# Optimization experiments

Measured on AMD Instinct MI355X. Metric: run time of the kernel, lower is better.

## Reference

```python
import jax, jax.numpy as jnp
import numpy as np

B, S, D = 1, 2048, 2048
E, K, F = 16, 4, 512
EPS = 1e-6


def setup_inputs() -> dict:
    key = jax.random.key(0)
    ks = jax.random.split(key, 5)
    return {
        "hidden_states": jax.random.normal(ks[0], (B, S, D), dtype=jnp.float32),
        "norm_weight": jnp.ones((D,), dtype=jnp.float32),
        "gate_w": jax.random.normal(ks[1], (E, D), dtype=jnp.float32) * 0.02,
        "w_gate": jax.random.normal(ks[2], (E, D, F), dtype=jnp.float32) * 0.02,
        "w_up": jax.random.normal(ks[3], (E, D, F), dtype=jnp.float32) * 0.02,
        "w_down": jax.random.normal(ks[4], (E, F, D), dtype=jnp.float32) * 0.02,
    }


def _rmsnorm(x, w, eps=EPS):
    xf = x.astype(jnp.float32)
    var = jnp.mean(xf * xf, axis=-1, keepdims=True)
    return (xf * jax.lax.rsqrt(var + eps)).astype(x.dtype) * w


def reference(hidden_states, norm_weight, gate_w, w_gate, w_up, w_down):
    residual = hidden_states
    h = _rmsnorm(hidden_states, norm_weight)
    x = h.reshape(-1, D)                                  # [T, D], T = B*S
    T = x.shape[0]

    # Router: softmax over experts (fp32), top-k, renormalize top-k weights.
    logits = x @ gate_w.T                                  # [T, E]
    probs = jax.nn.softmax(logits.astype(jnp.float32), axis=-1)
    top_w, top_i = jax.lax.top_k(probs, K)                 # [T, K]
    top_w = top_w / jnp.sum(top_w, axis=-1, keepdims=True)
    top_w = top_w.astype(x.dtype)

    # Dense combine matrix [T, E]: routing weight if selected, else 0.
    comb = jnp.zeros((T, E), dtype=x.dtype)
    comb = comb.at[jnp.arange(T)[:, None], top_i].add(top_w)

    # Experts: SiLU-gated MLP per expert, combined with routing weights.
    g = jnp.einsum("td,edf->tef", x, w_gate)               # [T, E, F]
    u = jnp.einsum("td,edf->tef", x, w_up)                 # [T, E, F]
    act = jax.nn.silu(g) * u                               # [T, E, F]
    # Weight per-expert contributions then project down.
    y = jnp.einsum("tef,efd,te->td", act, w_down, comb)    # [T, D]

    out = residual + y.reshape(B, S, D)
    return out
```

## Files before the change

### kernel.cpp

```cpp
#include <hip/hip_runtime.h>
#include <cstdint>
#include <cstddef>

#define T_ 2048
#define D_ 2048
#define E_ 16
#define F_ 512

typedef unsigned short u16;
typedef unsigned int u32;
typedef unsigned long long u64;
typedef __attribute__((ext_vector_type(8))) short bf16x8;
typedef __attribute__((ext_vector_type(4))) float f32x4;
typedef __attribute__((ext_vector_type(2))) u32 u32x2;
typedef __attribute__((ext_vector_type(4))) u32 u32x4;
typedef __attribute__((ext_vector_type(8))) u16 u16x8;

__device__ __forceinline__ u16 f2bf(float f){
  union { float f; u32 u; } c; c.f = f;
  return (u16)((c.u + 0x7FFFu + ((c.u >> 16) & 1u)) >> 16);
}

__device__ __forceinline__ void gload16(const void* g, void* l){
  __builtin_amdgcn_global_load_lds((const __attribute__((address_space(1))) void*)g,
                                   (__attribute__((address_space(3))) void*)l,
                                   16, 0, 0);
}

__device__ __forceinline__ u32 pk2(float a, float b){
  u32 r;
  asm("v_cvt_pk_bf16_f32 %0, %1, %2" : "=v"(r) : "v"(a), "v"(b));
  return r;
}

__global__ __launch_bounds__(256) void k_norm_router(
    const float* __restrict__ x, const float* __restrict__ nw, const float* __restrict__ gw,
    u16* __restrict__ h, int* __restrict__ tok_e, float* __restrict__ tok_w)
{
  const int t = blockIdx.x, tid = threadIdx.x;
  const int lane = tid & 63, wid = tid >> 6;
  const int d0 = tid * 8;
  const float4 v0 = *(const float4*)(x + (size_t)t*D_ + d0);
  const float4 v1 = *(const float4*)(x + (size_t)t*D_ + d0 + 4);
  float hv[8] = {v0.x, v0.y, v0.z, v0.w, v1.x, v1.y, v1.z, v1.w};
  float ss = 0.f;
  #pragma unroll
  for (int j = 0; j < 8; ++j) ss += hv[j]*hv[j];
  #pragma unroll
  for (int o = 32; o; o >>= 1) ss += __shfl_xor(ss, o);
  __shared__ float sred[4];
  __shared__ float red16[4][16];
  __shared__ float lf[16];
  if (lane == 0) sred[wid] = ss;
  __syncthreads();
  const float rstd = rsqrtf((sred[0]+sred[1]+sred[2]+sred[3]) * (1.f/(float)D_) + 1e-6f);
  const float4 w0 = *(const float4*)(nw + d0);
  const float4 w1 = *(const float4*)(nw + d0 + 4);
  const float wv[8] = {w0.x,w0.y,w0.z,w0.w,w1.x,w1.y,w1.z,w1.w};
  #pragma unroll
  for (int j = 0; j < 8; ++j) hv[j] = hv[j] * rstd * wv[j];
  u16x8 hb;
  #pragma unroll
  for (int j = 0; j < 8; ++j) hb[j] = f2bf(hv[j]);
  *(u16x8*)(h + (size_t)t*D_ + d0) = hb;

  float lg[16];
  #pragma unroll
  for (int e = 0; e < 16; ++e){
    const float4 g0 = *(const float4*)(gw + e*D_ + d0);
    const float4 g1 = *(const float4*)(gw + e*D_ + d0 + 4);
    lg[e] = hv[0]*g0.x + hv[1]*g0.y + hv[2]*g0.z + hv[3]*g0.w
          + hv[4]*g1.x + hv[5]*g1.y + hv[6]*g1.z + hv[7]*g1.w;
  }
  #pragma unroll
  for (int e = 0; e < 16; ++e){
    #pragma unroll
    for (int o = 32; o; o >>= 1) lg[e] += __shfl_xor(lg[e], o);
  }
  if (lane == 0){
    #pragma unroll
    for (int e = 0; e < 16; ++e) red16[wid][e] = lg[e];
  }
  __syncthreads();
  if (tid < 16) lf[tid] = red16[0][tid] + red16[1][tid] + red16[2][tid] + red16[3][tid];
  __syncthreads();
  if (tid == 0){
    float l[16];
    #pragma unroll
    for (int e = 0; e < 16; ++e) l[e] = lf[e];
    int sel[4]; float sv[4]; u32 used = 0;
    for (int k = 0; k < 4; ++k){
      float b = -3.4e38f; int bi = 0;
      for (int e = 0; e < 16; ++e)
        if (!((used >> e) & 1u) && l[e] > b){ b = l[e]; bi = e; }
      used |= 1u << bi; sel[k] = bi; sv[k] = b;
    }
    float ex[4]; float s = 0.f;
    for (int k = 0; k < 4; ++k){ ex[k] = __expf(sv[k] - sv[0]); s += ex[k]; }
    const float inv = 1.f / s;
    int4 te = {sel[0], sel[1], sel[2], sel[3]};
    float4 tw4 = {ex[0]*inv, ex[1]*inv, ex[2]*inv, ex[3]*inv};
    *(int4*)(tok_e + t*4) = te;
    *(float4*)(tok_w + t*4) = tw4;
  }
}

__global__ __launch_bounds__(256) void k_build_lists(
    const int* __restrict__ tok_e, const float* __restrict__ tok_w,
    int* __restrict__ eidx, float* __restrict__ ew, int* __restrict__ counts)
{
  const int e = blockIdx.x, tid = threadIdx.x;
  const int lane = tid & 63, wid = tid >> 6;
  __shared__ int wtot[4];
  __shared__ int base;
  if (tid == 0) base = 0;
  __syncthreads();
  for (int t0 = 0; t0 < T_; t0 += 256){
    const int t = t0 + tid;
    const int4 te = *(const int4*)(tok_e + t*4);
    const float4 tw = *(const float4*)(tok_w + t*4);
    bool m = false; float wv = 0.f;
    if      (te.x == e){ m = true; wv = tw.x; }
    else if (te.y == e){ m = true; wv = tw.y; }
    else if (te.z == e){ m = true; wv = tw.z; }
    else if (te.w == e){ m = true; wv = tw.w; }
    const u64 mask = __ballot(m);
    const int pre = __popcll(mask & ((1ull << lane) - 1ull));
    if (lane == 0) wtot[wid] = __popcll(mask);
    __syncthreads();
    int wbase = base;
    for (int i = 0; i < wid; ++i) wbase += wtot[i];
    if (m){
      eidx[e*T_ + wbase + pre] = t;
      ew[e*T_ + wbase + pre] = wv;
    }
    __syncthreads();
    if (tid == 0) base += wtot[0] + wtot[1] + wtot[2] + wtot[3];
    __syncthreads();
  }
  if (tid == 0) counts[e] = base;
}

__global__ __launch_bounds__(256) void k_slots(
    const int* __restrict__ counts, const int* __restrict__ eidx,
    const int* __restrict__ tok_e, int* __restrict__ tok_slot)
{
  const int e = blockIdx.x;
  int abase = 0;
  for (int i = 0; i < e; ++i) abase += counts[i];
  const int cnt = counts[e];
  for (int s = threadIdx.x; s < cnt; s += 256){
    const int t = eidx[e*T_ + s];
    const int4 te = *(const int4*)(tok_e + t*4);
    const int kidx = (te.x == e) ? 0 : (te.y == e) ? 1 : (te.z == e) ? 2 : 3;
    tok_slot[t*4 + kidx] = abase + s;
  }
}

#define WLOAD(KB, SRC, S) do {                                                 \
    _Pragma("unroll")                                                          \
    for (int j = 0; j < 2; ++j){                                               \
      const float4 t_ = *(const float4*)((SRC) + (size_t)((KB) + ko*2 + j)*(S));\
      wvf[0][j]=t_.x; wvf[1][j]=t_.y; wvf[2][j]=t_.z; wvf[3][j]=t_.w;          \
    }                                                                          \
  } while (0)

#define WSTORE(WP) do {                                                        \
    _Pragma("unroll")                                                          \
    for (int i = 0; i < 4; ++i){                                               \
      const int r_ = rg4*4 + i;                                                \
      const u32 idx_ = (u32)(r_*32 + ((ko>>2) ^ (r_&3) ^ ((r_>>2)&3))*8 + (ko&3)*2); \
      *(u32*)&(WP)[idx_] = pk2(wvf[i][0], wvf[i][1]);                          \
    }                                                                          \
  } while (0)

__global__ __launch_bounds__(256, 4) void k_gateup(
    const u16* __restrict__ h, const float* __restrict__ wg, const float* __restrict__ wu,
    const int* __restrict__ counts, const int* __restrict__ eidx, const float* __restrict__ ew,
    u16* __restrict__ act)
{
  const int bid = blockIdx.x;
  const int tt = bid >> 8;
  const int e  = (bid >> 4) & 15;
  const int ft = bid & 15;

  const int cnt = counts[e];
  const int row0 = tt * 256;
  if (row0 >= cnt) return;
  int abase = 0;
  for (int i = 0; i < e; ++i) abase += counts[i];

  const int tid = threadIdx.x, lane = tid & 63, w = tid >> 6;
  const int f0 = ft * 32;

  __shared__ __align__(16) u16 Xs[3][8192];
  __shared__ __align__(16) u16 Ws[2][2048];

  int* toksS = (int*)&Xs[0][0];
  if (tid < 256){
    const int slot = row0 + tid;
    const int cs = slot < cnt ? slot : (cnt - 1);
    toksS[tid] = eidx[e*T_ + cs];
  }
  __syncthreads();

  const int lr = lane >> 2, lc = lane & 3;
  const int csw = lc ^ (lr & 3) ^ ((lr >> 2) & 3);
  const u16* srcX[4]; u32 dof[4];
  #pragma unroll
  for (int q = 0; q < 4; ++q){
    const int r = w*64 + q*16 + lr;
    srcX[q] = h + (size_t)toksS[r]*D_ + 8*csw;
    dof[q] = (u32)((w*64 + q*16) * 32);
  }
  const int rg4 = tid & 15, ko = tid >> 4;
  const float* wsel = (rg4 < 8) ? wg : wu;
  const float* srcWf = wsel + (size_t)e*D_*F_ + f0 + ((rg4*4) & 31);
  __syncthreads();

  const int p = lane & 15, g4 = lane >> 4;
  u32 aB[4], bB[4];
  #pragma unroll
  for (int m = 0; m < 4; ++m) aB[m] = (u32)((w*64 + m*16 + p) * 32);
  #pragma unroll
  for (int n = 0; n < 4; ++n) bB[n] = (u32)((n*16 + p) * 32);
  const u32 s8 = 8u * (u32)(g4 ^ (p & 3) ^ ((p >> 2) & 3));

  f32x4 acc[4][4] = {};
  float wvf[4][2];

  WLOAD(0, srcWf, F_);
  #pragma unroll
  for (int q = 0; q < 4; ++q) gload16(srcX[q],      (void*)&Xs[0][dof[q]]);
  #pragma unroll
  for (int q = 0; q < 4; ++q) gload16(srcX[q] + 32, (void*)&Xs[1][dof[q]]);
  asm volatile("s_waitcnt vmcnt(8)" ::: "memory");
  __builtin_amdgcn_sched_barrier(0);
  WSTORE(&Ws[0][0]);
  asm volatile("s_waitcnt vmcnt(4)" ::: "memory");

  const int NSTEP = D_ / 32;
  int xc = 0;
  for (int kt = 0; kt < NSTEP; ++kt){
    asm volatile("s_waitcnt lgkmcnt(0)" ::: "memory");
    __builtin_amdgcn_s_barrier();
    __builtin_amdgcn_sched_barrier(0);
    if (kt + 1 < NSTEP){
      WLOAD((kt + 1) * 32, srcWf, F_);
      __builtin_amdgcn_sched_barrier(0);
    }
    {
      const u16* Xp = &Xs[xc][0];
      const u16* Wp = &Ws[kt & 1][0];
      bf16x8 aF[4], bF[4];
      #pragma unroll
      for (int m = 0; m < 4; ++m) aF[m] = *(const bf16x8*)&Xp[aB[m] + s8];
      #pragma unroll
      for (int n = 0; n < 4; ++n) bF[n] = *(const bf16x8*)&Wp[bB[n] + s8];
      #pragma unroll
      for (int m = 0; m < 4; ++m)
        #pragma unroll
        for (int n = 0; n < 4; ++n)
          acc[m][n] = __builtin_amdgcn_mfma_f32_16x16x32_bf16(aF[m], bF[n], acc[m][n], 0, 0, 0);
    }
    if (kt + 2 < NSTEP){
      const int kb2 = (kt + 2) * 32;
      int nb = xc + 2; if (nb >= 3) nb -= 3;
      #pragma unroll
      for (int q = 0; q < 4; ++q) gload16(srcX[q] + kb2, (void*)&Xs[nb][dof[q]]);
    }
    if (kt + 1 < NSTEP){
      if (kt + 2 < NSTEP) asm volatile("s_waitcnt vmcnt(4)" ::: "memory");
      else                asm volatile("s_waitcnt vmcnt(0)" ::: "memory");
      __builtin_amdgcn_sched_barrier(0);
      WSTORE(&Ws[(kt + 1) & 1][0]);
    }
    xc = (xc == 2) ? 0 : xc + 1;
  }

  #pragma unroll
  for (int m = 0; m < 4; ++m)
    #pragma unroll
    for (int r = 0; r < 4; ++r){
      const int row  = w*64 + m*16 + g4*4 + r;
      const int slot = row0 + row;
      if (slot < cnt){
        const float tw = ew[e*T_ + slot];
        #pragma unroll
        for (int n = 0; n < 2; ++n){
          const float gv = acc[m][n][r], uv = acc[m][n+2][r];
          const float a = tw * (gv / (1.f + __expf(-gv))) * uv;
          act[(size_t)(abase + slot)*F_ + f0 + n*16 + p] = f2bf(a);
        }
      }
    }
}

__global__ __launch_bounds__(512, 4) void k_down(
    const u16* __restrict__ act, const float* __restrict__ wd,
    const int* __restrict__ counts, u16* __restrict__ ydown)
{
  const int bid = blockIdx.x;
  const int tt = bid >> 8;
  const int e  = (bid >> 4) & 15;
  const int dt = bid & 15;

  const int cnt = counts[e], row0 = tt * 256;
  if (row0 >= cnt) return;
  int abase = 0;
  for (int i = 0; i < e; ++i) abase += counts[i];

  const int tid = threadIdx.x, lane = tid & 63, w = tid >> 6;
  const int d0 = dt * 128;

  __shared__ __align__(16) u16 As[3][8192];
  __shared__ __align__(16) u16 Wd[2][4096];

  const int lr = lane >> 2, lc = lane & 3;
  const int csw = lc ^ (lr & 3) ^ ((lr >> 2) & 3);
  const u16* srcX[2]; u32 dof[2];
  #pragma unroll
  for (int q = 0; q < 2; ++q){
    const int r = w*32 + q*16 + lr;
    const int rs = (row0 + r < cnt) ? (row0 + r) : (cnt - 1);
    srcX[q] = act + (size_t)(abase + rs)*F_ + 8*csw;
    dof[q] = (u32)((w*32 + q*16) * 32);
  }
  const int rg4 = tid & 31, ko = tid >> 5;
  const float* srcWf = wd + (size_t)e*F_*D_ + d0 + rg4*4;

  const int p = lane & 15, g4 = lane >> 4;
  const int tm = w >> 1, dh = w & 1;
  u32 aB[4], bB[4];
  #pragma unroll
  for (int m = 0; m < 4; ++m) aB[m] = (u32)((tm*64 + m*16 + p) * 32);
  #pragma unroll
  for (int n = 0; n < 4; ++n) bB[n] = (u32)((dh*64 + n*16 + p) * 32);
  const u32 s8 = 8u * (u32)(g4 ^ (p & 3) ^ ((p >> 2) & 3));

  f32x4 acc[4][4] = {};
  float wvf[4][2];

  WLOAD(0, srcWf, D_);
  #pragma unroll
  for (int q = 0; q < 2; ++q) gload16(srcX[q],      (void*)&As[0][dof[q]]);
  #pragma unroll
  for (int q = 0; q < 2; ++q) gload16(srcX[q] + 32, (void*)&As[1][dof[q]]);
  asm volatile("s_waitcnt vmcnt(4)" ::: "memory");
  __builtin_amdgcn_sched_barrier(0);
  WSTORE(&Wd[0][0]);
  asm volatile("s_waitcnt vmcnt(2)" ::: "memory");

  const int NSTEP = F_ / 32;
  int xc = 0;
  for (int kt = 0; kt < NSTEP; ++kt){
    asm volatile("s_waitcnt lgkmcnt(0)" ::: "memory");
    __builtin_amdgcn_s_barrier();
    __builtin_amdgcn_sched_barrier(0);
    if (kt + 1 < NSTEP){
      WLOAD((kt + 1) * 32, srcWf, D_);
      __builtin_amdgcn_sched_barrier(0);
    }
    {
      const u16* Ap = &As[xc][0];
      const u16* Wp = &Wd[kt & 1][0];
      bf16x8 aF[4], bF[4];
      #pragma unroll
      for (int m = 0; m < 4; ++m) aF[m] = *(const bf16x8*)&Ap[aB[m] + s8];
      #pragma unroll
      for (int n = 0; n < 4; ++n) bF[n] = *(const bf16x8*)&Wp[bB[n] + s8];
      #pragma unroll
      for (int m = 0; m < 4; ++m)
        #pragma unroll
        for (int n = 0; n < 4; ++n)
          acc[m][n] = __builtin_amdgcn_mfma_f32_16x16x32_bf16(aF[m], bF[n], acc[m][n], 0, 0, 0);
    }
    if (kt + 2 < NSTEP){
      const int kb2 = (kt + 2) * 32;
      int nb = xc + 2; if (nb >= 3) nb -= 3;
      #pragma unroll
      for (int q = 0; q < 2; ++q) gload16(srcX[q] + kb2, (void*)&As[nb][dof[q]]);
    }
    if (kt + 1 < NSTEP){
      if (kt + 2 < NSTEP) asm volatile("s_waitcnt vmcnt(2)" ::: "memory");
      else                asm volatile("s_waitcnt vmcnt(0)" ::: "memory");
      __builtin_amdgcn_sched_barrier(0);
      WSTORE(&Wd[(kt + 1) & 1][0]);
    }
    xc = (xc == 2) ? 0 : xc + 1;
  }

  #pragma unroll
  for (int m = 0; m < 4; ++m){
    #pragma unroll
    for (int r = 0; r < 4; ++r){
      const int row  = tm*64 + m*16 + g4*4 + r;
      const int slot = row0 + row;
      if (slot < cnt){
        u16* yp = ydown + (size_t)(abase + slot)*D_ + d0 + dh*64;
        #pragma unroll
        for (int n = 0; n < 4; ++n)
          yp[n*16 + p] = f2bf(acc[m][n][r]);
      }
    }
  }
}

__global__ __launch_bounds__(256) void k_combine(
    const float* __restrict__ x, const u16* __restrict__ ydown,
    const int* __restrict__ tok_slot, float* __restrict__ out)
{
  const int t = blockIdx.x;
  const int d0 = threadIdx.x * 8;
  const int4 sl = *(const int4*)(tok_slot + t*4);
  const float4 x0 = *(const float4*)(x + (size_t)t*D_ + d0);
  const float4 x1 = *(const float4*)(x + (size_t)t*D_ + d0 + 4);
  float s[8] = {x0.x, x0.y, x0.z, x0.w, x1.x, x1.y, x1.z, x1.w};
  const int sls[4] = {sl.x, sl.y, sl.z, sl.w};
  #pragma unroll
  for (int k = 0; k < 4; ++k){
    const u16x8 v = *(const u16x8*)(ydown + (size_t)sls[k]*D_ + d0);
    #pragma unroll
    for (int j = 0; j < 8; ++j){
      union { u32 u; float f; } c; c.u = (u32)v[j] << 16;
      s[j] += c.f;
    }
  }
  float4 o0 = {s[0], s[1], s[2], s[3]};
  float4 o1 = {s[4], s[5], s[6], s[7]};
  *(float4*)(out + (size_t)t*D_ + d0)     = o0;
  *(float4*)(out + (size_t)t*D_ + d0 + 4) = o1;
}

extern "C" void kernel_launch(void* const* d_in, const int* in_sizes, int n_in,
                              void* d_out, int out_size, void* d_ws, size_t ws_size,
                              hipStream_t stream)
{
  (void)in_sizes; (void)n_in; (void)out_size; (void)ws_size;
  const float* x     = (const float*)d_in[0];
  const float* nw    = (const float*)d_in[1];
  const float* gw    = (const float*)d_in[2];
  const float* wgate = (const float*)d_in[3];
  const float* wup   = (const float*)d_in[4];
  const float* wdown = (const float*)d_in[5];
  float* out = (float*)d_out;

  char* ws = (char*)d_ws;
  u16*   h        = (u16*)(ws);
  u16*   act      = (u16*)(ws + 8388608);
  int*   counts   = (int*)(ws + 16908288);
  int*   eidx     = (int*)(ws + 16908352);
  float* ew       = (float*)(ws + 17039424);
  int*   tok_e    = (int*)(ws + 17170496);
  float* tok_w    = (float*)(ws + 17203264);
  int*   tok_slot = (int*)(ws + 17236032);
  u16*   ydown    = (u16*)(ws + 17268800);

  k_norm_router<<<T_, 256, 0, stream>>>(x, nw, gw, h, tok_e, tok_w);
  k_build_lists<<<E_, 256, 0, stream>>>(tok_e, tok_w, eidx, ew, counts);
  k_slots<<<E_, 256, 0, stream>>>(counts, eidx, tok_e, tok_slot);
  k_gateup<<<2048, 256, 0, stream>>>(h, wgate, wup, counts, eidx, ew, act);
  k_down<<<2048, 512, 0, stream>>>(act, wdown, counts, ydown);
  k_combine<<<T_, 256, 0, stream>>>(x, ydown, tok_slot, out);
}
```

Measured before the change: 205.0 us.

## Widen gate/up tile to 64 F-columns with 8-wave blocks

The gate/up kernel now uses 512-thread blocks that each cover 256 tokens by 64 F columns (gate and up), with warps split 4x2 over rows and F halves. This halves the number of blocks and the gathered activation rows loaded per output column, so each X tile in shared memory is reused across twice as many weight columns. The weight tile buffer doubles, and each thread issues fewer X gathers per step. The trade-off is fewer blocks in flight and higher per-block shared memory, which may lower occupancy. The load/store macros are renamed, with no change in behavior.

```diff
diff --git a/kernel.cpp b/kernel.cpp
--- a/kernel.cpp
+++ b/kernel.cpp
@@ -157,7 +157,7 @@
   }
 }
 
-#define WLOAD(KB, SRC, S) do {                                                 \
+#define WLOADD(KB, SRC, S) do {                                                \
     _Pragma("unroll")                                                          \
     for (int j = 0; j < 2; ++j){                                               \
       const float4 t_ = *(const float4*)((SRC) + (size_t)((KB) + ko*2 + j)*(S));\
@@ -165,7 +165,7 @@
     }                                                                          \
   } while (0)
 
-#define WSTORE(WP) do {                                                        \
+#define WSTORED(WP) do {                                                       \
     _Pragma("unroll")                                                          \
     for (int i = 0; i < 4; ++i){                                               \
       const int r_ = rg4*4 + i;                                                \
@@ -174,15 +174,15 @@
     }                                                                          \
   } while (0)
 
-__global__ __launch_bounds__(256, 4) void k_gateup(
+__global__ __launch_bounds__(512, 4) void k_gateup(
     const u16* __restrict__ h, const float* __restrict__ wg, const float* __restrict__ wu,
     const int* __restrict__ counts, const int* __restrict__ eidx, const float* __restrict__ ew,
     u16* __restrict__ act)
 {
   const int bid = blockIdx.x;
-  const int tt = bid >> 8;
-  const int e  = (bid >> 4) & 15;
-  const int ft = bid & 15;
+  const int tt = bid >> 7;
+  const int e  = (bid >> 3) & 15;
+  const int ft = bid & 7;
 
   const int cnt = counts[e];
   const int row0 = tt * 256;
@@ -191,10 +191,10 @@
   for (int i = 0; i < e; ++i) abase += counts[i];
 
   const int tid = threadIdx.x, lane = tid & 63, w = tid >> 6;
-  const int f0 = ft * 32;
+  const int f0 = ft * 64;
 
   __shared__ __align__(16) u16 Xs[3][8192];
-  __shared__ __align__(16) u16 Ws[2][2048];
+  __shared__ __align__(16) u16 Ws[2][4096];
 
   int* toksS = (int*)&Xs[0][0];
   if (tid < 256){
@@ -206,38 +206,42 @@
 
   const int lr = lane >> 2, lc = lane & 3;
   const int csw = lc ^ (lr & 3) ^ ((lr >> 2) & 3);
-  const u16* srcX[4]; u32 dof[4];
-  #pragma unroll
-  for (int q = 0; q < 4; ++q){
-    const int r = w*64 + q*16 + lr;
+  const u16* srcX[2]; u32 dof[2];
+  #pragma unroll
+  for (int q = 0; q < 2; ++q){
+    const int r = w*32 + q*16 + lr;
     srcX[q] = h + (size_t)toksS[r]*D_ + 8*csw;
-    dof[q] = (u32)((w*64 + q*16) * 32);
-  }
-  const int rg4 = tid & 15, ko = tid >> 4;
-  const float* wsel = (rg4 < 8) ? wg : wu;
-  const float* srcWf = wsel + (size_t)e*D_*F_ + f0 + ((rg4*4) & 31);
+    dof[q] = (u32)((w*32 + q*16) * 32);
+  }
+  const int rg4 = tid & 31, ko = tid >> 5;
+  const float* wsel = (rg4 < 16) ? wg : wu;
+  const float* srcWf = wsel + (size_t)e*D_*F_ + f0 + ((rg4*4) & 63);
   __syncthreads();
 
   const int p = lane & 15, g4 = lane >> 4;
+  const int tm = w >> 1, fh = w & 1;
   u32 aB[4], bB[4];
   #pragma unroll
-  for (int m = 0; m < 4; ++m) aB[m] = (u32)((w*64 + m*16 + p) * 32);
-  #pragma unroll
-  for (int n = 0; n < 4; ++n) bB[n] = (u32)((n*16 + p) * 32);
+  for (int m = 0; m < 4; ++m) aB[m] = (u32)((tm*64 + m*16 + p) * 32);
+  #pragma unroll
+  for (int n = 0; n < 2; ++n){
+    bB[n]   = (u32)((     fh*32 + n*16 + p) * 32);
+    bB[n+2] = (u32)((64 + fh*32 + n*16 + p) * 32);
+  }
   const u32 s8 = 8u * (u32)(g4 ^ (p & 3) ^ ((p >> 2) & 3));
 
   f32x4 acc[4][4] = {};
   float wvf[4][2];
 
-  WLOAD(0, srcWf, F_);
-  #pragma unroll
-  for (int q = 0; q < 4; ++q) gload16(srcX[q],      (void*)&Xs[0][dof[q]]);
-  #pragma unroll
-  for (int q = 0; q < 4; ++q) gload16(srcX[q] + 32, (void*)&Xs[1][dof[q]]);
-  asm volatile("s_waitcnt vmcnt(8)" ::: "memory");
+  WLOADD(0, srcWf, F_);
+  #pragma unroll
+  for (int q = 0; q < 2; ++q) gload16(srcX[q],      (void*)&Xs[0][dof[q]]);
+  #pragma unroll
+  for (int q = 0; q < 2; ++q) gload16(srcX[q] + 32, (void*)&Xs[1][dof[q]]);
+  asm volatile("s_waitcnt vmcnt(4)" ::: "memory");
   __builtin_amdgcn_sched_barrier(0);
-  WSTORE(&Ws[0][0]);
-  asm volatile("s_waitcnt vmcnt(4)" ::: "memory");
+  WSTORED(&Ws[0][0]);
+  asm volatile("s_waitcnt vmcnt(2)" ::: "memory");
 
   const int NSTEP = D_ / 32;
   int xc = 0;
@@ -246,7 +250,7 @@
     __builtin_amdgcn_s_barrier();
     __builtin_amdgcn_sched_barrier(0);
     if (kt + 1 < NSTEP){
-      WLOAD((kt + 1) * 32, srcWf, F_);
+      WLOADD((kt + 1) * 32, srcWf, F_);
       __builtin_amdgcn_sched_barrier(0);
     }
     {
@@ -267,13 +271,13 @@
       const int kb2 = (kt + 2) * 32;
       int nb = xc + 2; if (nb >= 3) nb -= 3;
       #pragma unroll
-      for (int q = 0; q < 4; ++q) gload16(srcX[q] + kb2, (void*)&Xs[nb][dof[q]]);
+      for (int q = 0; q < 2; ++q) gload16(srcX[q] + kb2, (void*)&Xs[nb][dof[q]]);
     }
     if (kt + 1 < NSTEP){
-      if (kt + 2 < NSTEP) asm volatile("s_waitcnt vmcnt(4)" ::: "memory");
+      if (kt + 2 < NSTEP) asm volatile("s_waitcnt vmcnt(2)" ::: "memory");
       else                asm volatile("s_waitcnt vmcnt(0)" ::: "memory");
       __builtin_amdgcn_sched_barrier(0);
-      WSTORE(&Ws[(kt + 1) & 1][0]);
+      WSTORED(&Ws[(kt + 1) & 1][0]);
     }
     xc = (xc == 2) ? 0 : xc + 1;
   }
@@ -282,7 +286,7 @@
   for (int m = 0; m < 4; ++m)
     #pragma unroll
     for (int r = 0; r < 4; ++r){
-      const int row  = w*64 + m*16 + g4*4 + r;
+      const int row  = tm*64 + m*16 + g4*4 + r;
       const int slot = row0 + row;
       if (slot < cnt){
         const float tw = ew[e*T_ + slot];
@@ -290,7 +294,7 @@
         for (int n = 0; n < 2; ++n){
           const float gv = acc[m][n][r], uv = acc[m][n+2][r];
           const float a = tw * (gv / (1.f + __expf(-gv))) * uv;
-          act[(size_t)(abase + slot)*F_ + f0 + n*16 + p] = f2bf(a);
+          act[(size_t)(abase + slot)*F_ + f0 + fh*32 + n*16 + p] = f2bf(a);
         }
       }
     }
@@ -341,14 +345,14 @@
   f32x4 acc[4][4] = {};
   float wvf[4][2];
 
-  WLOAD(0, srcWf, D_);
+  WLOADD(0, srcWf, D_);
   #pragma unroll
   for (int q = 0; q < 2; ++q) gload16(srcX[q],      (void*)&As[0][dof[q]]);
   #pragma unroll
   for (int q = 0; q < 2; ++q) gload16(srcX[q] + 32, (void*)&As[1][dof[q]]);
   asm volatile("s_waitcnt vmcnt(4)" ::: "memory");
   __builtin_amdgcn_sched_barrier(0);
-  WSTORE(&Wd[0][0]);
+  WSTORED(&Wd[0][0]);
   asm volatile("s_waitcnt vmcnt(2)" ::: "memory");
 
   const int NSTEP = F_ / 32;
@@ -358,7 +362,7 @@
     __builtin_amdgcn_s_barrier();
     __builtin_amdgcn_sched_barrier(0);
     if (kt + 1 < NSTEP){
-      WLOAD((kt + 1) * 32, srcWf, D_);
+      WLOADD((kt + 1) * 32, srcWf, D_);
       __builtin_amdgcn_sched_barrier(0);
     }
     {
@@ -385,7 +389,7 @@
       if (kt + 2 < NSTEP) asm volatile("s_waitcnt vmcnt(2)" ::: "memory");
       else                asm volatile("s_waitcnt vmcnt(0)" ::: "memory");
       __builtin_amdgcn_sched_barrier(0);
-      WSTORE(&Wd[(kt + 1) & 1][0]);
+      WSTORED(&Wd[(kt + 1) & 1][0]);
     }
     xc = (xc == 2) ? 0 : xc + 1;
   }
@@ -459,7 +463,7 @@
   k_norm_router<<<T_, 256, 0, stream>>>(x, nw, gw, h, tok_e, tok_w);
   k_build_lists<<<E_, 256, 0, stream>>>(tok_e, tok_w, eidx, ew, counts);
   k_slots<<<E_, 256, 0, stream>>>(counts, eidx, tok_e, tok_slot);
-  k_gateup<<<2048, 256, 0, stream>>>(h, wgate, wup, counts, eidx, ew, act);
+  k_gateup<<<1024, 512, 0, stream>>>(h, wgate, wup, counts, eidx, ew, act);
   k_down<<<2048, 512, 0, stream>>>(act, wdown, counts, ydown);
   k_combine<<<T_, 256, 0, stream>>>(x, ydown, tok_slot, out);
 }
```

New measurement: 182.5 us. 11.0% less time.
